# Kernel tuning notes

Measured on AMD Instinct MI355X. Metric: run time of the kernel, lower is better.

Reference implementation:

```python
import jax, jax.numpy as jnp
import numpy as np

B, T, H, E, V = 128, 400, 512, 128, 50000
EPS = 1e-12


def setup_inputs() -> dict:
    key = jax.random.key(0)
    ks = jax.random.split(key, 20)
    n = lambda i, shape, s=0.02: (jax.random.normal(ks[i], shape, jnp.float32) * s)
    return dict(
        y_t_1=jax.random.randint(ks[0], (B,), 0, V),
        h0=n(1, (B, H), 0.1), c0=n(2, (B, H), 0.1),
        c_t_1=n(3, (B, 2 * H), 0.1),
        encoder_outputs=n(4, (B, T, 2 * H), 0.1),
        encoder_feature=n(5, (B, T, 2 * H), 0.1),
        mask_select=jnp.ones((B, T), jnp.float32),
        enc_batch_extend_vocab=jax.random.randint(ks[6], (B, T), 0, V),
        coverage=jnp.zeros((B, T), jnp.float32),
        emb_table=n(7, (V, E)),
        W_c=n(8, (2 * H, 1)),
        W_dp=n(9, (2 * H, 2 * H)), b_dp=jnp.zeros((2 * H,), jnp.float32),
        v_w=n(10, (1, 2 * H)),
        W_xc=n(11, (E, 2 * H + E)), b_xc=jnp.zeros((E,), jnp.float32),
        W_ih=n(12, (4 * H, E)), W_hh=n(13, (4 * H, H)),
        b_ih=jnp.zeros((4 * H,), jnp.float32), b_hh=jnp.zeros((4 * H,), jnp.float32),
        W_pg=n(14, (1, 4 * H + E)), b_pg=jnp.zeros((1,), jnp.float32),
        W_o1=n(15, (H, 3 * H)), b_o1=jnp.zeros((H,), jnp.float32),
        W_o2=n(16, (V, H)), b_o2=jnp.zeros((V,), jnp.float32),
    )


def reference(y_t_1, h0, c0, c_t_1, encoder_outputs, encoder_feature, mask_select,
              enc_batch_extend_vocab, coverage, emb_table, W_c, W_dp, b_dp, v_w,
              W_xc, b_xc, W_ih, W_hh, b_ih, b_hh, W_pg, b_pg, W_o1, b_o1, W_o2, b_o2):
    # embedding lookup + input context projection
    y_emb = emb_table[y_t_1]                                  # [B,E]
    x = jnp.concatenate([c_t_1, y_emb], axis=1) @ W_xc.T + b_xc  # [B,E]

    # single-step LSTM (torch gate order i,f,g,o)
    gates = x @ W_ih.T + b_ih + h0 @ W_hh.T + b_hh            # [B,4H]
    i, f, g, o = jnp.split(gates, 4, axis=1)
    c = jax.nn.sigmoid(f) * c0 + jax.nn.sigmoid(i) * jnp.tanh(g)
    h = jax.nn.sigmoid(o) * jnp.tanh(c)                       # lstm_out == h
    s_t_hat = jnp.concatenate([h, c], axis=1)                 # [B,2H]

    # Bahdanau attention with coverage
    dec_fea = s_t_hat @ W_dp.T + b_dp                         # [B,2H]
    cov_feat = coverage[..., None] * W_c[:, 0]                # [B,T,2H]
    e = jnp.tanh(encoder_feature + dec_fea[:, None, :] + cov_feat)
    scores = jnp.einsum('btn,n->bt', e, v_w[0])               # [B,T]
    attn_ = jax.nn.softmax(scores, axis=1) * mask_select
    attn = attn_ / (attn_.sum(axis=1, keepdims=True) + EPS)   # [B,T]
    c_t = jnp.einsum('bt,btn->bn', attn, encoder_outputs)     # [B,2H]
    coverage_next = coverage + attn

    # pointer-generator gate
    p_gen = jax.nn.sigmoid(jnp.concatenate([c_t, s_t_hat, x], axis=1) @ W_pg.T + b_pg)  # [B,1]

    # vocab distribution
    out = (jnp.concatenate([h, c_t], axis=1) @ W_o1.T + b_o1) @ W_o2.T + b_o2  # [B,V]
    vocab_dist = jax.nn.softmax(out, axis=1)

    # pointer mixing via scatter-add into vocab dist
    rows = jnp.arange(vocab_dist.shape[0])[:, None]
    final_dist = (p_gen * vocab_dist).at[rows, enc_batch_extend_vocab].add((1.0 - p_gen) * attn)
    return final_dist, h, c, c_t, attn, p_gen, coverage_next
```

## Files before the change

kernel.cpp:

```cpp
#include <hip/hip_runtime.h>
#include <hip/hip_bf16.h>
#include <cstdint>

#define B 128
#define T 400
#define H 512
#define H2 1024
#define H4 2048
#define E 128
#define V 50000
#define KPG 2176
#define EPSF 1e-12f

#define OFF_FIN 0
#define OFF_H   (B*V)
#define OFF_C   (OFF_H + B*H)
#define OFF_CT  (OFF_C + B*H)
#define OFF_AT  (OFF_CT + B*H2)
#define OFF_PG  (OFF_AT + B*T)
#define OFF_COV (OFF_PG + B)

struct IOb {
  using OT = __hip_bfloat16;
  static __device__ __forceinline__ bool want(const float* fl){ return fl[0] > 0.5f; }
  static __device__ __forceinline__ float ld(const void* p, size_t i){
    return __uint_as_float(((unsigned)((const unsigned short*)p)[i]) << 16);
  }
  static __device__ __forceinline__ void ld8(const void* p, size_t i, float* f){
    uint4 u = *reinterpret_cast<const uint4*>((const unsigned short*)p + i);
    f[0]=__uint_as_float(u.x<<16); f[1]=__uint_as_float(u.x&0xffff0000u);
    f[2]=__uint_as_float(u.y<<16); f[3]=__uint_as_float(u.y&0xffff0000u);
    f[4]=__uint_as_float(u.z<<16); f[5]=__uint_as_float(u.z&0xffff0000u);
    f[6]=__uint_as_float(u.w<<16); f[7]=__uint_as_float(u.w&0xffff0000u);
  }
  static __device__ __forceinline__ void ld4(const void* p, size_t i, float* f){
    uint2 u = *reinterpret_cast<const uint2*>((const unsigned short*)p + i);
    f[0]=__uint_as_float(u.x<<16); f[1]=__uint_as_float(u.x&0xffff0000u);
    f[2]=__uint_as_float(u.y<<16); f[3]=__uint_as_float(u.y&0xffff0000u);
  }
  static __device__ __forceinline__ void st(void* p, size_t i, float v){
    ((__hip_bfloat16*)p)[i] = __float2bfloat16(v);
  }
  static __device__ __forceinline__ void st8(void* p, size_t i, const float* f){
    __hip_bfloat16 h[8];
    #pragma unroll
    for(int j=0;j<8;j++) h[j]=__float2bfloat16(f[j]);
    *reinterpret_cast<uint4*>((__hip_bfloat16*)p + i) = *reinterpret_cast<const uint4*>(h);
  }
};
struct IOf {
  using OT = float;
  static __device__ __forceinline__ bool want(const float* fl){ return fl[0] < 0.5f; }
  static __device__ __forceinline__ float ld(const void* p, size_t i){
    return ((const float*)p)[i];
  }
  static __device__ __forceinline__ void ld8(const void* p, size_t i, float* f){
    const float* q = (const float*)p + i;
    float4 a = *reinterpret_cast<const float4*>(q);
    float4 b = *reinterpret_cast<const float4*>(q+4);
    f[0]=a.x; f[1]=a.y; f[2]=a.z; f[3]=a.w;
    f[4]=b.x; f[5]=b.y; f[6]=b.z; f[7]=b.w;
  }
  static __device__ __forceinline__ void ld4(const void* p, size_t i, float* f){
    float4 a = *reinterpret_cast<const float4*>((const float*)p + i);
    f[0]=a.x; f[1]=a.y; f[2]=a.z; f[3]=a.w;
  }
  static __device__ __forceinline__ void st(void* p, size_t i, float v){
    ((float*)p)[i] = v;
  }
  static __device__ __forceinline__ void st8(void* p, size_t i, const float* f){
    float* q = (float*)p + i;
    *reinterpret_cast<float4*>(q)   = make_float4(f[0],f[1],f[2],f[3]);
    *reinterpret_cast<float4*>(q+4) = make_float4(f[4],f[5],f[6],f[7]);
  }
};

__device__ __forceinline__ float ftanh(float x){
  x = fminf(10.f, fmaxf(-10.f, x));
  float a = __expf(2.f*x);
  return 1.f - 2.f/(a+1.f);
}
__device__ __forceinline__ float fsig(float x){ return 1.f/(1.f+__expf(-x)); }

__device__ __forceinline__ float waveSum(float v){
  #pragma unroll
  for(int o=32;o>0;o>>=1) v += __shfl_down(v,o);
  return v;
}
__device__ __forceinline__ float waveMax(float v){
  #pragma unroll
  for(int o=32;o>0;o>>=1) v = fmaxf(v,__shfl_down(v,o));
  return v;
}

__device__ __forceinline__ void ldf8(const float* p, float* f){
  float4 a = *reinterpret_cast<const float4*>(p);
  float4 b = *reinterpret_cast<const float4*>(p+4);
  f[0]=a.x; f[1]=a.y; f[2]=a.z; f[3]=a.w;
  f[4]=b.x; f[5]=b.y; f[6]=b.z; f[7]=b.w;
}
__device__ __forceinline__ void stf8(float* p, const float* f){
  *reinterpret_cast<float4*>(p)   = make_float4(f[0],f[1],f[2],f[3]);
  *reinterpret_cast<float4*>(p+4) = make_float4(f[4],f[5],f[6],f[7]);
}

__global__ void k_detect(const void* mask, float* flagp){
  if(blockIdx.x==0 && threadIdx.x==0){
    unsigned u = *(const unsigned*)mask;
    flagp[0] = (((u>>16)==0x3F80u) && ((u&0xFFFFu)==0x3F80u)) ? 1.f : 0.f;
  }
}

__global__ void k_zero4(float4* p, int n){
  int i = blockIdx.x*256+threadIdx.x; if(i<n) p[i]=make_float4(0.f,0.f,0.f,0.f);
}

template<class IO>
__global__ void k_prep0(const float* flag, const int* y, const void* c_t_1, const void* emb, float* A0){
  if(!IO::want(flag)) return;
  int b = blockIdx.x, tid = threadIdx.x;
  float f[8];
  if(tid < 128){
    IO::ld8(c_t_1, (size_t)b*H2 + tid*8, f);
    stf8(A0 + (size_t)b*1152 + tid*8, f);
  } else if(tid < 144){
    int yb = y[b];
    IO::ld8(emb, (size_t)yb*E + (tid-128)*8, f);
    stf8(A0 + (size_t)b*1152 + H2 + (tid-128)*8, f);
  }
}

template<class IO>
__global__ void k_prep_h(const float* flag, const void* h0, float* A1){
  if(!IO::want(flag)) return;
  int t = blockIdx.x*256 + threadIdx.x;
  int n = (t*8)&511, b = (t*8)>>9;
  float f[8];
  IO::ld8(h0, (size_t)b*H + n, f);
  stf8(A1 + (size_t)b*640 + E + n, f);
}

template<class IO>
__global__ __launch_bounds__(256) void k_gemm(const float* flag, const float* A, int lda,
    const void* W0, int K0, const void* W1, int K1,
    const void* bias, float* C, int ldc, int CH){
  if(!IO::want(flag)) return;
  __shared__ float as[32][66];
  __shared__ float wsm[32][36];
  int tid = threadIdx.x;
  int j0 = blockIdx.x*32;
  int b0 = blockIdx.y*64;
  int kz = blockIdx.z;
  int bq = tid & 31, jg = tid >> 5;
  float acc[2][4];
  #pragma unroll
  for(int i=0;i<2;i++){
    #pragma unroll
    for(int jj=0;jj<4;jj++) acc[i][jj]=0.f;
  }
  int arow = tid>>2, ac = (tid&3)*8;

  for(int ci=0; ci<CH; ci++){
    int k0 = (kz*CH + ci)*32;
    __syncthreads();
    {
      const float* p = A + (size_t)(b0 + arow)*lda + k0 + ac;
      float4 q0 = *reinterpret_cast<const float4*>(p);
      float4 q1 = *reinterpret_cast<const float4*>(p+4);
      as[ac+0][arow]=q0.x; as[ac+1][arow]=q0.y; as[ac+2][arow]=q0.z; as[ac+3][arow]=q0.w;
      as[ac+4][arow]=q1.x; as[ac+5][arow]=q1.y; as[ac+6][arow]=q1.z; as[ac+7][arow]=q1.w;
    }
    if(tid < 128){
      const void* Wp; int st, kr;
      if(k0 < K0){ Wp=W0; st=K0; kr=k0; } else { Wp=W1; st=K1; kr=k0-K0; }
      int wrow = tid>>2, wc = (tid&3)*8;
      float f[8]; IO::ld8(Wp, (size_t)(j0+wrow)*st + kr + wc, f);
      #pragma unroll
      for(int i=0;i<8;i++) wsm[wc+i][wrow] = f[i];
    }
    __syncthreads();
    #pragma unroll
    for(int kk=0; kk<32; kk++){
      float2 a = *reinterpret_cast<const float2*>(&as[kk][bq*2]);
      float4 w = *reinterpret_cast<const float4*>(&wsm[kk][jg*4]);
      acc[0][0] += a.x*w.x; acc[0][1] += a.x*w.y; acc[0][2] += a.x*w.z; acc[0][3] += a.x*w.w;
      acc[1][0] += a.y*w.x; acc[1][1] += a.y*w.y; acc[1][2] += a.y*w.z; acc[1][3] += a.y*w.w;
    }
  }
  if(kz==0 && bias){
    #pragma unroll
    for(int jj=0;jj<4;jj++){
      float bv = IO::ld(bias, j0 + jg*4 + jj);
      acc[0][jj] += bv; acc[1][jj] += bv;
    }
  }
  #pragma unroll
  for(int i=0;i<2;i++){
    float* cp = C + (size_t)(b0 + bq*2 + i)*ldc + j0 + jg*4;
    atomicAdd(cp+0, acc[i][0]); atomicAdd(cp+1, acc[i][1]);
    atomicAdd(cp+2, acc[i][2]); atomicAdd(cp+3, acc[i][3]);
  }
}

template<class IO>
__global__ void k_cell(const float* flag, const float* gts, const void* c0,
                       const void* b_ih, const void* b_hh,
                       float* A2, float* A3, void* dout){
  if(!IO::want(flag)) return;
  int t = blockIdx.x*256 + threadIdx.x;
  int n = (t*8)&511, b = (t*8)>>9;
  size_t gb = (size_t)b*H4 + n;
  float gi[8],gf[8],gg[8],go[8],c0v[8];
  ldf8(gts+gb,        gi); ldf8(gts+gb+H,   gf);
  ldf8(gts+gb+2*H,    gg); ldf8(gts+gb+3*H, go);
  float bi0[8],bi1[8],bi2[8],bi3[8],bh0[8],bh1[8],bh2[8],bh3[8];
  IO::ld8(b_ih, n, bi0); IO::ld8(b_ih, H+n, bi1); IO::ld8(b_ih, 2*H+n, bi2); IO::ld8(b_ih, 3*H+n, bi3);
  IO::ld8(b_hh, n, bh0); IO::ld8(b_hh, H+n, bh1); IO::ld8(b_hh, 2*H+n, bh2); IO::ld8(b_hh, 3*H+n, bh3);
  IO::ld8(c0, (size_t)b*H + n, c0v);
  float hv[8], cv[8];
  #pragma unroll
  for(int j=0;j<8;j++){
    float ig = fsig (gi[j]+bi0[j]+bh0[j]);
    float fg = fsig (gf[j]+bi1[j]+bh1[j]);
    float gv = ftanh(gg[j]+bi2[j]+bh2[j]);
    float og = fsig (go[j]+bi3[j]+bh3[j]);
    float c = fg*c0v[j] + ig*gv;
    cv[j]=c; hv[j]=og*ftanh(c);
  }
  stf8(A2 + (size_t)b*H2 + n,     hv);
  stf8(A2 + (size_t)b*H2 + H + n, cv);
  stf8(A3 + (size_t)b*1536 + n,   hv);
  IO::st8(dout, (size_t)OFF_H + (size_t)b*H + n, hv);
  IO::st8(dout, (size_t)OFF_C + (size_t)b*H + n, cv);
}

template<class IO>
__global__ void k_scores(const float* flag, const void* enc_feat, const float* ws_dec,
                         const void* W_c, const void* v_w, const void* coverage,
                         float* ws_scores){
  if(!IO::want(flag)) return;
  int blk = blockIdx.x;
  int b  = blk / (T/16);
  int tb = (blk % (T/16))*16;
  int tid = threadIdx.x;
  int wave = tid >> 6, lane = tid & 63;
  int n0 = lane*16;
  float dec[16], wc[16], vw[16];
  #pragma unroll
  for(int i=0;i<16;i+=4){
    float4 v4 = *reinterpret_cast<const float4*>(ws_dec + b*H2 + n0 + i);
    dec[i]=v4.x; dec[i+1]=v4.y; dec[i+2]=v4.z; dec[i+3]=v4.w;
  }
  IO::ld8(W_c, n0, wc); IO::ld8(W_c, n0+8, wc+8);
  IO::ld8(v_w, n0, vw); IO::ld8(v_w, n0+8, vw+8);
  #pragma unroll
  for(int it=0; it<4; ++it){
    int t = tb + wave*4 + it;
    float cov = IO::ld(coverage, (size_t)b*T + t);
    size_t base = ((size_t)b*T + t)*H2 + n0;
    float ef[16]; IO::ld8(enc_feat, base, ef); IO::ld8(enc_feat, base+8, ef+8);
    float sum=0.f;
    #pragma unroll
    for(int i=0;i<16;i++){
      float s = ef[i] + dec[i] + cov*wc[i];
      sum += ftanh(s)*vw[i];
    }
    sum = waveSum(sum);
    if(lane==0) ws_scores[b*T + t] = sum;
  }
}

template<class IO>
__global__ void k_attn(const float* flag, const float* ws_scores, const void* mask,
                       const void* coverage, float* ws_attn, void* dout){
  if(!IO::want(flag)) return;
  __shared__ float red[8];
  __shared__ float bc0, bc1, bc2;
  int b=blockIdx.x, tid=threadIdx.x;
  int lane = tid & 63, w = tid >> 6;
  float s = (tid<T)? ws_scores[b*T+tid] : -3.0e38f;
  float m = waveMax(s);
  if(lane==0) red[w]=m;
  __syncthreads();
  if(tid==0){ float v=red[0]; for(int i=1;i<8;i++)v=fmaxf(v,red[i]); bc0=v; }
  __syncthreads();
  float e = (tid<T)? __expf(s-bc0) : 0.f;
  float sm = waveSum(e);
  if(lane==0) red[w]=sm;
  __syncthreads();
  if(tid==0){ float v=0; for(int i=0;i<8;i++)v+=red[i]; bc1=v; }
  __syncthreads();
  float attn_ = (tid<T)? (e/bc1)*IO::ld(mask, (size_t)b*T+tid) : 0.f;
  float s2 = waveSum(attn_);
  if(lane==0) red[w]=s2;
  __syncthreads();
  if(tid==0){ float v=0; for(int i=0;i<8;i++)v+=red[i]; bc2=v; }
  __syncthreads();
  float attn = attn_/(bc2+EPSF);
  if(tid<T){
    ws_attn[b*T+tid]=attn;
    IO::st(dout, (size_t)OFF_AT + b*T+tid, attn);
    IO::st(dout, (size_t)OFF_COV + b*T+tid, IO::ld(coverage,(size_t)b*T+tid)+attn);
  }
}

template<class IO>
__global__ void k_ctx(const float* flag, const void* enc_out, const float* ws_attn, float* A3){
  if(!IO::want(flag)) return;
  __shared__ float at[50];
  int b = blockIdx.x>>3, ch = blockIdx.x&7, tid=threadIdx.x;
  if(tid<50) at[tid] = ws_attn[b*T + ch*50 + tid];
  __syncthreads();
  int n0 = tid*4;
  float a0=0,a1=0,a2=0,a3=0;
  size_t base = ((size_t)b*T + ch*50)*H2 + n0;
  for(int t=0;t<50;t++){
    float a = at[t];
    float f[4]; IO::ld4(enc_out, base, f);
    a0 += a*f[0]; a1 += a*f[1]; a2 += a*f[2]; a3 += a*f[3];
    base += H2;
  }
  float* cp = A3 + (size_t)b*1536 + H + n0;
  atomicAdd(cp+0, a0); atomicAdd(cp+1, a1);
  atomicAdd(cp+2, a2); atomicAdd(cp+3, a3);
}

template<class IO>
__global__ void k_pgen(const float* flag, const float* A1, const float* A2, const float* A3,
                       const void* W_pg, const void* b_pg, float* ws_pg, void* dout){
  if(!IO::want(flag)) return;
  __shared__ float red[4];
  int b=blockIdx.x, tid=threadIdx.x;
  int lane = tid&63, w = tid>>6;
  float part=0.f;
  for(int k=tid;k<KPG;k+=256){
    float xv;
    if(k<H2)            xv = A3[(size_t)b*1536 + H + k];
    else if(k<H2+H)     xv = A2[(size_t)b*H2 + (k-H2)];
    else if(k<2*H2)     xv = A2[(size_t)b*H2 + H + (k-H2-H)];
    else                xv = A1[(size_t)b*640 + (k-2*H2)];
    part += xv * IO::ld(W_pg, k);
  }
  part = waveSum(part);
  if(lane==0) red[w]=part;
  __syncthreads();
  if(tid==0){
    float v = red[0]+red[1]+red[2]+red[3] + IO::ld(b_pg, 0);
    float pg = fsig(v);
    ws_pg[b]=pg;
    IO::st(dout, (size_t)OFF_PG + b, pg);
  }
  for(int k=tid;k<H2;k+=256) IO::st(dout, (size_t)OFF_CT + b*H2+k, A3[(size_t)b*1536 + H + k]);
}

template<class IO>
__global__ __launch_bounds__(256) void k_logits(const float* flag, const float* ws_o1,
                                                const void* W_o2, const void* b_o2,
                                                float* ws_logits){
  if(!IO::want(flag)) return;
  __shared__ float o1s[32][132];
  __shared__ float wvs[32][68];
  int v0 = blockIdx.x * 64;
  int tid = threadIdx.x;
  int bg = tid & 31;
  int vg = tid >> 5;
  float acc[4][8];
  #pragma unroll
  for(int i=0;i<4;i++){
    #pragma unroll
    for(int j=0;j<8;j++) acc[i][j]=0.f; }
  for(int k0=0;k0<H;k0+=32){
    __syncthreads();
    {
      int bb = tid>>1, kc = (tid&1)*16;
      const float* q = ws_o1 + bb*H + k0 + kc;
      float4 q0 = *reinterpret_cast<const float4*>(q);
      float4 q1 = *reinterpret_cast<const float4*>(q+4);
      float4 q2 = *reinterpret_cast<const float4*>(q+8);
      float4 q3 = *reinterpret_cast<const float4*>(q+12);
      o1s[kc+ 0][bb]=q0.x; o1s[kc+ 1][bb]=q0.y; o1s[kc+ 2][bb]=q0.z; o1s[kc+ 3][bb]=q0.w;
      o1s[kc+ 4][bb]=q1.x; o1s[kc+ 5][bb]=q1.y; o1s[kc+ 6][bb]=q1.z; o1s[kc+ 7][bb]=q1.w;
      o1s[kc+ 8][bb]=q2.x; o1s[kc+ 9][bb]=q2.y; o1s[kc+10][bb]=q2.z; o1s[kc+11][bb]=q2.w;
      o1s[kc+12][bb]=q3.x; o1s[kc+13][bb]=q3.y; o1s[kc+14][bb]=q3.z; o1s[kc+15][bb]=q3.w;
    }
    {
      int vv = tid>>2, c = (tid&3)*8;
      int v = v0+vv; bool ok = (v<V);
      float f[8]; IO::ld8(W_o2, (size_t)(ok? v : (V-1))*H + k0 + c, f);
      #pragma unroll
      for(int j=0;j<8;j++) wvs[c+j][vv] = ok? f[j] : 0.f;
    }
    __syncthreads();
    #pragma unroll 8
    for(int kk=0;kk<32;kk++){
      float4 a  = *reinterpret_cast<const float4*>(&o1s[kk][bg*4]);
      float4 w0 = *reinterpret_cast<const float4*>(&wvs[kk][vg*8]);
      float4 w1 = *reinterpret_cast<const float4*>(&wvs[kk][vg*8+4]);
      float av[4]={a.x,a.y,a.z,a.w};
      float wv[8]={w0.x,w0.y,w0.z,w0.w,w1.x,w1.y,w1.z,w1.w};
      #pragma unroll
      for(int i=0;i<4;i++){
        #pragma unroll
        for(int j=0;j<8;j++) acc[i][j] += av[i]*wv[j];
      }
    }
  }
  #pragma unroll
  for(int i=0;i<4;i++){
    int bb = bg*4+i;
    #pragma unroll
    for(int j=0;j<8;j++){
      int v = v0 + vg*8 + j;
      if(v<V) ws_logits[(size_t)bb*V + v] = acc[i][j] + IO::ld(b_o2, v);
    }
  }
}

__global__ void k_vsoft(const float* lg, const float* pg, float* fin){
  __shared__ float red[4];
  __shared__ float bcast;
  int b=blockIdx.x, tid=threadIdx.x;
  int lane = tid&63, w = tid>>6;
  float m=-3.0e38f;
  for(int v=tid; v<V; v+=256) m = fmaxf(m, lg[(size_t)b*V+v]);
  m = waveMax(m);
  if(lane==0) red[w]=m;
  __syncthreads();
  if(tid==0) bcast = fmaxf(fmaxf(red[0],red[1]),fmaxf(red[2],red[3]));
  __syncthreads();
  float mx = bcast;
  float s=0.f;
  for(int v=tid; v<V; v+=256) s += __expf(lg[(size_t)b*V+v]-mx);
  s = waveSum(s);
  if(lane==0) red[w]=s;
  __syncthreads();
  if(tid==0) bcast = red[0]+red[1]+red[2]+red[3];
  __syncthreads();
  float scale = pg[b] / bcast;
  for(int v=tid; v<V; v+=256) fin[(size_t)b*V+v] = __expf(lg[(size_t)b*V+v]-mx)*scale;
}

__global__ void k_scatter(const int* ext, const float* ws_attn, const float* ws_pg, float* ws_final){
  int i = blockIdx.x*256+threadIdx.x;
  if(i>=B*T) return;
  int b=i/T;
  float add = (1.f-ws_pg[b])*ws_attn[i];
  atomicAdd(&ws_final[(size_t)b*V + ext[i]], add);
}

template<class IO>
__global__ void k_tostore(const float* flag, const float* src, void* dout, int n8){
  if(!IO::want(flag)) return;
  int i = blockIdx.x*256+threadIdx.x;
  if(i>=n8) return;
  size_t off = (size_t)i*8;
  float f[8];
  ldf8(src + off, f);
  IO::st8(dout, (size_t)OFF_FIN + off, f);
}

extern "C" void kernel_launch(void* const* d_in, const int* in_sizes, int n_in,
                              void* d_out, int out_size, void* d_ws, size_t ws_size,
                              hipStream_t stream){
  const int* y_t_1 = (const int*)d_in[0];
  const void* h0   =d_in[1];  const void* c0   =d_in[2];  const void* c_t_1=d_in[3];
  const void* enc_out=d_in[4]; const void* enc_feat=d_in[5]; const void* mask=d_in[6];
  const int* ext = (const int*)d_in[7];
  const void* coverage=d_in[8]; const void* emb=d_in[9];  const void* W_c=d_in[10];
  const void* W_dp=d_in[11];   const void* b_dp=d_in[12]; const void* v_w=d_in[13];
  const void* W_xc=d_in[14];   const void* b_xc=d_in[15];
  const void* W_ih=d_in[16];   const void* W_hh=d_in[17];
  const void* b_ih=d_in[18];   const void* b_hh=d_in[19];
  const void* W_pg=d_in[20];   const void* b_pg=d_in[21];
  const void* W_o1=d_in[22];   const void* b_o1=d_in[23];
  const void* W_o2=d_in[24];   const void* b_o2=d_in[25];

  float* ws = (float*)d_ws;
  float* ws_A1  = ws;
  float* ws_dec = ws_A1  + 128*640;
  float* ws_o1  = ws_dec + 128*1024;
  float* ws_A3  = ws_o1  + 128*512;
  float* ws_A2  = ws_A3  + 128*1536;
  float* ws_sc  = ws_A2  + 128*1024;
  float* ws_attn= ws_sc  + B*T;
  float* ws_pg  = ws_attn+ B*T;
  float* ws_log = ws_pg  + B;
  float* ws_gates = ws_log;
  float* ws_A0    = ws_log + 128*2048;
  float* ws_flag  = ws_log + (size_t)B*V;

  k_detect<<<dim3(1), dim3(64), 0, stream>>>(mask, ws_flag);
  k_zero4 <<<dim3(464), dim3(256), 0, stream>>>((float4*)ws, 118784);
  k_zero4 <<<dim3(256), dim3(256), 0, stream>>>((float4*)ws_gates, 65536);

  k_prep0<IOb><<<dim3(B), dim3(192), 0, stream>>>(ws_flag, y_t_1, c_t_1, emb, ws_A0);
  k_prep0<IOf><<<dim3(B), dim3(192), 0, stream>>>(ws_flag, y_t_1, c_t_1, emb, ws_A0);
  k_prep_h<IOb><<<dim3(32), dim3(256), 0, stream>>>(ws_flag, h0, ws_A1);
  k_prep_h<IOf><<<dim3(32), dim3(256), 0, stream>>>(ws_flag, h0, ws_A1);

  k_gemm<IOb><<<dim3(4,2,12), dim3(256), 0, stream>>>(ws_flag, ws_A0, 1152, W_xc, 1152, nullptr, 0, b_xc, ws_A1, 640, 3);
  k_gemm<IOf><<<dim3(4,2,12), dim3(256), 0, stream>>>(ws_flag, ws_A0, 1152, W_xc, 1152, nullptr, 0, b_xc, ws_A1, 640, 3);

  k_gemm<IOb><<<dim3(64,2,2), dim3(256), 0, stream>>>(ws_flag, ws_A1, 640, W_ih, E, W_hh, H, nullptr, ws_gates, H4, 10);
  k_gemm<IOf><<<dim3(64,2,2), dim3(256), 0, stream>>>(ws_flag, ws_A1, 640, W_ih, E, W_hh, H, nullptr, ws_gates, H4, 10);

  k_cell<IOb><<<dim3(32), dim3(256), 0, stream>>>(ws_flag, ws_gates, c0, b_ih, b_hh, ws_A2, ws_A3, d_out);
  k_cell<IOf><<<dim3(32), dim3(256), 0, stream>>>(ws_flag, ws_gates, c0, b_ih, b_hh, ws_A2, ws_A3, d_out);

  k_gemm<IOb><<<dim3(32,2,4), dim3(256), 0, stream>>>(ws_flag, ws_A2, H2, W_dp, H2, nullptr, 0, b_dp, ws_dec, H2, 8);
  k_gemm<IOf><<<dim3(32,2,4), dim3(256), 0, stream>>>(ws_flag, ws_A2, H2, W_dp, H2, nullptr, 0, b_dp, ws_dec, H2, 8);

  k_scores<IOb><<<dim3(B*(T/16)), dim3(256), 0, stream>>>(ws_flag, enc_feat, ws_dec, W_c, v_w, coverage, ws_sc);
  k_scores<IOf><<<dim3(B*(T/16)), dim3(256), 0, stream>>>(ws_flag, enc_feat, ws_dec, W_c, v_w, coverage, ws_sc);

  k_attn<IOb><<<dim3(B), dim3(512), 0, stream>>>(ws_flag, ws_sc, mask, coverage, ws_attn, d_out);
  k_attn<IOf><<<dim3(B), dim3(512), 0, stream>>>(ws_flag, ws_sc, mask, coverage, ws_attn, d_out);

  k_ctx<IOb><<<dim3(B*8), dim3(256), 0, stream>>>(ws_flag, enc_out, ws_attn, ws_A3);
  k_ctx<IOf><<<dim3(B*8), dim3(256), 0, stream>>>(ws_flag, enc_out, ws_attn, ws_A3);

  k_pgen<IOb><<<dim3(B), dim3(256), 0, stream>>>(ws_flag, ws_A1, ws_A2, ws_A3, W_pg, b_pg, ws_pg, d_out);
  k_pgen<IOf><<<dim3(B), dim3(256), 0, stream>>>(ws_flag, ws_A1, ws_A2, ws_A3, W_pg, b_pg, ws_pg, d_out);

  k_gemm<IOb><<<dim3(16,2,8), dim3(256), 0, stream>>>(ws_flag, ws_A3, 1536, W_o1, 1536, nullptr, 0, b_o1, ws_o1, H, 6);
  k_gemm<IOf><<<dim3(16,2,8), dim3(256), 0, stream>>>(ws_flag, ws_A3, 1536, W_o1, 1536, nullptr, 0, b_o1, ws_o1, H, 6);

  k_logits<IOb><<<dim3((V+63)/64), dim3(256), 0, stream>>>(ws_flag, ws_o1, W_o2, b_o2, ws_log);
  k_logits<IOf><<<dim3((V+63)/64), dim3(256), 0, stream>>>(ws_flag, ws_o1, W_o2, b_o2, ws_log);

  k_vsoft   <<<dim3(B), dim3(256), 0, stream>>>(ws_log, ws_pg, ws_log);
  k_scatter <<<dim3((B*T+255)/256), dim3(256), 0, stream>>>(ext, ws_attn, ws_pg, ws_log);

  k_tostore<IOb><<<dim3((B*V/8+255)/256), dim3(256), 0, stream>>>(ws_flag, ws_log, d_out, B*V/8);
  k_tostore<IOf><<<dim3((B*V/8+255)/256), dim3(256), 0, stream>>>(ws_flag, ws_log, d_out, B*V/8);
}
```

Before: 946.3 us.

## Split vocab softmax into chunked partial reductions, combine, and scale kernels

New measurement: 825.5 us. 1.15x faster.

```diff
diff --git a/kernel.cpp b/kernel.cpp
--- a/kernel.cpp
+++ b/kernel.cpp
@@ -11,6 +11,8 @@
 #define V 50000
 #define KPG 2176
 #define EPSF 1e-12f
+#define VCH 25
+#define VCHUNK 2000
 
 #define OFF_FIN 0
 #define OFF_H   (B*V)
@@ -416,28 +418,64 @@
   }
 }
 
-__global__ void k_vsoft(const float* lg, const float* pg, float* fin){
+__global__ void k_vred(const float* lg, float* pm){
   __shared__ float red[4];
-  __shared__ float bcast;
-  int b=blockIdx.x, tid=threadIdx.x;
+  __shared__ float bcm;
+  int b = blockIdx.x / VCH, ch = blockIdx.x % VCH;
+  int tid = threadIdx.x;
   int lane = tid&63, w = tid>>6;
-  float m=-3.0e38f;
-  for(int v=tid; v<V; v+=256) m = fmaxf(m, lg[(size_t)b*V+v]);
+  bool act = tid < (VCHUNK/8);
+  float f[8];
+  float m = -3.0e38f;
+  if(act){
+    ldf8(lg + (size_t)b*V + ch*VCHUNK + tid*8, f);
+    #pragma unroll
+    for(int j=0;j<8;j++) m = fmaxf(m, f[j]);
+  }
   m = waveMax(m);
   if(lane==0) red[w]=m;
   __syncthreads();
-  if(tid==0) bcast = fmaxf(fmaxf(red[0],red[1]),fmaxf(red[2],red[3]));
-  __syncthreads();
-  float mx = bcast;
-  float s=0.f;
-  for(int v=tid; v<V; v+=256) s += __expf(lg[(size_t)b*V+v]-mx);
+  if(tid==0) bcm = fmaxf(fmaxf(red[0],red[1]),fmaxf(red[2],red[3]));
+  __syncthreads();
+  float mx = bcm;
+  float s = 0.f;
+  if(act){
+    #pragma unroll
+    for(int j=0;j<8;j++) s += __expf(f[j]-mx);
+  }
   s = waveSum(s);
   if(lane==0) red[w]=s;
   __syncthreads();
-  if(tid==0) bcast = red[0]+red[1]+red[2]+red[3];
-  __syncthreads();
-  float scale = pg[b] / bcast;
-  for(int v=tid; v<V; v+=256) fin[(size_t)b*V+v] = __expf(lg[(size_t)b*V+v]-mx)*scale;
+  if(tid==0){
+    float sv = red[0]+red[1]+red[2]+red[3];
+    pm[(b*VCH+ch)*2+0] = mx;
+    pm[(b*VCH+ch)*2+1] = sv;
+  }
+}
+
+__global__ void k_vcomb(const float* pm, const float* pg, float* mxsc){
+  int b = blockIdx.x, tid = threadIdx.x;
+  float m = (tid<VCH)? pm[(b*VCH+tid)*2+0] : -3.0e38f;
+  float M = waveMax(m);
+  M = __shfl(M, 0);
+  float s = (tid<VCH)? pm[(b*VCH+tid)*2+1]*__expf(m-M) : 0.f;
+  s = waveSum(s);
+  if(tid==0){
+    mxsc[b*2+0] = M;
+    mxsc[b*2+1] = pg[b]/s;
+  }
+}
+
+__global__ void k_vscale(const float* lg, const float* mxsc, float* fin){
+  int i = blockIdx.x*256 + threadIdx.x;
+  if(i >= B*(V/8)) return;
+  int b = i / (V/8);
+  size_t off = (size_t)b*V + (size_t)(i - b*(V/8))*8;
+  float mx = mxsc[b*2+0], sc = mxsc[b*2+1];
+  float f[8]; ldf8(lg+off, f);
+  #pragma unroll
+  for(int j=0;j<8;j++) f[j] = __expf(f[j]-mx)*sc;
+  stf8(fin+off, f);
 }
 
 __global__ void k_scatter(const int* ext, const float* ws_attn, const float* ws_pg, float* ws_final){
@@ -488,6 +526,8 @@
   float* ws_gates = ws_log;
   float* ws_A0    = ws_log + 128*2048;
   float* ws_flag  = ws_log + (size_t)B*V;
+  float* ws_pm    = ws_sc;
+  float* ws_mxsc  = ws_sc + 2*B*VCH;
 
   k_detect<<<dim3(1), dim3(64), 0, stream>>>(mask, ws_flag);
   k_zero4 <<<dim3(464), dim3(256), 0, stream>>>((float4*)ws, 118784);
@@ -528,7 +568,10 @@
   k_logits<IOb><<<dim3((V+63)/64), dim3(256), 0, stream>>>(ws_flag, ws_o1, W_o2, b_o2, ws_log);
   k_logits<IOf><<<dim3((V+63)/64), dim3(256), 0, stream>>>(ws_flag, ws_o1, W_o2, b_o2, ws_log);
 
-  k_vsoft   <<<dim3(B), dim3(256), 0, stream>>>(ws_log, ws_pg, ws_log);
+  k_vred  <<<dim3(B*VCH), dim3(256), 0, stream>>>(ws_log, ws_pm);
+  k_vcomb <<<dim3(B), dim3(64), 0, stream>>>(ws_pm, ws_pg, ws_mxsc);
+  k_vscale<<<dim3(B*(V/8)/256), dim3(256), 0, stream>>>(ws_log, ws_mxsc, ws_log);
+
   k_scatter <<<dim3((B*T+255)/256), dim3(256), 0, stream>>>(ext, ws_attn, ws_pg, ws_log);
 
   k_tostore<IOb><<<dim3((B*V/8+255)/256), dim3(256), 0, stream>>>(ws_flag, ws_log, d_out, B*V/8);
```
